# Performance work log

Measured on AMD Instinct MI355X. Metric: run time of the kernel, lower is better.

Reference implementation:

```python
import jax, jax.numpy as jnp
import numpy as np

N_HEAD = 12
TOP_M = 16
MIN_SIZE = 2
MAX_SIZE = 8
ALPHA = 1.0
EPS = 1e-6

# Note: in the torch source, minimize_det=True and minimize_det=False select the
# identical subset (the sign flip in the score is exactly undone by flipping the
# comparisons), so we implement the single equivalent rule: maximize
# s = -log(det(K_S K_S^T) + 1e-6) / |S|**alpha.

def _token(qi, i, k_all, v_all):
    """Greedy DPP subset selection for one query token i. qi:[d], k_all/v_all:[T,d]."""
    T, d = k_all.shape
    slots = jnp.arange(MAX_SIZE)
    sim = k_all @ qi
    sim = jnp.where(jnp.arange(T) <= i, sim, -jnp.inf)  # causal mask
    vals, topidx = jax.lax.top_k(sim, TOP_M)
    avail0 = jnp.isfinite(vals) & (topidx != i)  # i is removed from candidates
    k_cand = k_all[topidx]                        # [M,d]
    cand_norm = jnp.sum(k_cand * k_cand, axis=-1)  # [M]
    ki = k_all[i]
    sel0 = jnp.zeros((MAX_SIZE,), jnp.int32).at[0].set(i.astype(jnp.int32))
    s0 = jax.lax.stop_gradient(-jnp.log(jnp.dot(ki, ki) + EPS))  # |S|=1 => size^alpha=1

    def body(state, _):
        sel, count, cur_s, avail, done = state
        # E: selected key vectors in slots < count, zeros elsewhere
        E = jnp.where((slots < count)[:, None], k_all[sel], 0.0)  # [S,d]
        G0 = E @ E.T                                              # [S,S]
        cross = k_cand @ E.T  # [M,S]; column `count` is 0 since that E row is 0
        u = (slots == count).astype(E.dtype)  # one-hot insertion slot
        # Gram of S u {c} for every candidate c, identity-padded beyond slot count
        grams = (G0[None]
                 + u[None, :, None] * cross[:, None, :]
                 + cross[:, :, None] * u[None, None, :]
                 + cand_norm[:, None, None] * (u[:, None] * u[None, :])[None])
        grams = grams + jnp.diag(jnp.where(slots > count, 1.0, 0.0))[None]
        det = jnp.linalg.det(grams.astype(jnp.float32))  # [M]
        s = -jnp.log(det + EPS) / (count + 1).astype(jnp.float32) ** ALPHA
        s = jax.lax.stop_gradient(jnp.where(avail, s, -jnp.inf))
        best = jnp.argmax(s)
        best_s = s[best]
        accept = (~done) & jnp.any(avail) & ((best_s > cur_s) | (count < MIN_SIZE))
        sel = jnp.where(accept & (slots == count), topidx[best].astype(jnp.int32), sel)
        avail = avail & ~(accept & (jnp.arange(TOP_M) == best))
        cur_s = jnp.where(accept, best_s, cur_s)
        count = count + accept.astype(count.dtype)
        done = done | ~accept
        return (sel, count, cur_s, avail, done), None

    init = (sel0, jnp.int32(1), s0, avail0, jnp.bool_(False))
    (sel, count, _, _, _), _ = jax.lax.scan(body, init, None, length=MAX_SIZE - 1)
    w = (slots < count).astype(v_all.dtype)
    return (v_all[sel] * w[:, None]).sum(0) / count.astype(v_all.dtype)

_tokens = jax.vmap(_token, in_axes=(0, 0, None, None))  # over T

def _head(qh, kh, vh):
    return _tokens(qh, jnp.arange(qh.shape[0]), kh, vh)

_attn = jax.vmap(jax.vmap(_head))  # over B, H

def _forward(x, W_attn, b_attn, W_proj, b_proj):
    B, T, C = x.shape
    hs = C // N_HEAD
    qkv = x @ W_attn + b_attn
    q, k, v = jnp.split(qkv, 3, axis=-1)
    q = q.reshape(B, T, N_HEAD, hs).transpose(0, 2, 1, 3)
    k = k.reshape(B, T, N_HEAD, hs).transpose(0, 2, 1, 3)
    v = v.reshape(B, T, N_HEAD, hs).transpose(0, 2, 1, 3)
    y = _attn(q, k, v)  # [B,H,T,hs]
    y = y.transpose(0, 2, 1, 3).reshape(B, T, C)
    return y @ W_proj + b_proj  # dropout=0.0 (eval)

def setup_inputs():
    key = jax.random.key(0)
    ks = jax.random.split(key, 3)
    B, T, C = 4, 512, 768
    return {
        "x": jax.random.normal(ks[0], (B, T, C), jnp.float32),
        "W_attn": jax.random.normal(ks[1], (C, 3 * C), jnp.float32) * 0.02,
        "b_attn": jnp.zeros((3 * C,), jnp.float32),
        "W_proj": jax.random.normal(ks[2], (C, C), jnp.float32) * 0.02,
        "b_proj": jnp.zeros((C,), jnp.float32),
    }

def reference(x, W_attn, b_attn, W_proj, b_proj):
    return _forward(x, W_attn, b_attn, W_proj, b_proj)
```

## Files before the change

### kernel.cpp

```cpp
#include <hip/hip_runtime.h>
#include <math.h>

constexpr int Bc = 4, Tc = 512, Cc = 768, Hc = 12, HSc = 64;
constexpr int QKVN = 3 * Cc;
constexpr double EPSd = 1e-6;

typedef unsigned short u16;
typedef __attribute__((ext_vector_type(8))) short short8;
typedef __attribute__((ext_vector_type(4))) float f32x4;

__device__ __forceinline__ u16 f2bf(float x) {
  unsigned u = __float_as_uint(x);
  return (u16)((u + 0x7FFFu + ((u >> 16) & 1u)) >> 16);
}
__device__ __forceinline__ float bf2f(u16 h) {
  return __uint_as_float((unsigned)h << 16);
}

__device__ __forceinline__ void gload16(const u16* g, u16* l) {
  __builtin_amdgcn_global_load_lds(
      (const __attribute__((address_space(1))) void*)g,
      (__attribute__((address_space(3))) void*)l, 16, 0, 0);
}

#define WAITVM6 asm volatile("s_waitcnt vmcnt(6)" ::: "memory")
#define WAITVM0 asm volatile("s_waitcnt vmcnt(0)" ::: "memory")

__global__ void __launch_bounds__(256) convsplit3(
    const float* __restrict__ in, u16* __restrict__ H, u16* __restrict__ M,
    u16* __restrict__ L) {
  const int i = blockIdx.x * 256 + threadIdx.x;
  const float4 v = ((const float4*)in)[i];
  const float x[4] = {v.x, v.y, v.z, v.w};
  ushort4 hv, mv, lv;
  u16* hp = (u16*)&hv; u16* mp = (u16*)&mv; u16* lp = (u16*)&lv;
#pragma unroll
  for (int c = 0; c < 4; ++c) {
    const u16 h = f2bf(x[c]);
    const float r1 = x[c] - bf2f(h);
    const u16 m = f2bf(r1);
    const u16 l = f2bf(r1 - bf2f(m));
    hp[c] = h; mp[c] = m; lp[c] = l;
  }
  ((ushort4*)H)[i] = hv;
  ((ushort4*)M)[i] = mv;
  ((ushort4*)L)[i] = lv;
}

__global__ void __launch_bounds__(256) convsplit3_t(
    const float* __restrict__ W, u16* __restrict__ Th, u16* __restrict__ Tm,
    u16* __restrict__ Tl, int K, int Nn) {
  __shared__ float t[64][65];
  const int k0 = blockIdx.x * 64, n0 = blockIdx.y * 64;
#pragma unroll
  for (int u = 0; u < 16; ++u) {
    const int idx = u * 256 + threadIdx.x;
    const int r = idx >> 6, c = idx & 63;
    t[r][c] = W[(size_t)(k0 + r) * Nn + n0 + c];
  }
  __syncthreads();
#pragma unroll
  for (int u = 0; u < 16; ++u) {
    const int idx = u * 256 + threadIdx.x;
    const int n = idx >> 6, k = idx & 63;
    const float x = t[k][n];
    const u16 h = f2bf(x);
    const float r1 = x - bf2f(h);
    const u16 m = f2bf(r1);
    const u16 l = f2bf(r1 - bf2f(m));
    Th[(size_t)(n0 + n) * K + k0 + k] = h;
    Tm[(size_t)(n0 + n) * K + k0 + k] = m;
    Tl[(size_t)(n0 + n) * K + k0 + k] = l;
  }
}

template <bool WRITE_PARTIAL>
__global__ void __launch_bounds__(256, 3) gemm_mfma3(
    const u16* __restrict__ A, const u16* __restrict__ B,
    const float* __restrict__ bias, float* __restrict__ outp,
    int N, int kPerSplit, int strideA, int strideB) {
  __shared__ __align__(16) u16 AsF[2][3 * 64 * 32];
  __shared__ __align__(16) u16 BsF[2][3 * 64 * 32];
  const int tid = threadIdx.x;
  const int wid = tid >> 6;
  const int lane = tid & 63;
  const int lm = lane & 15, kg = lane >> 4;
  const int wr = wid >> 1, wc = wid & 1;
  const int rb = blockIdx.x * 64;
  const int cb = blockIdx.y * 64;
  const int kBeg = blockIdx.z * kPerSplit;

  const int trow = tid >> 2;
  const int tc4 = tid & 3;
  const int krot = ((tc4 - (trow >> 1)) & 3) * 8;
  const int sLds = tid * 8;
  int aOff = (rb + trow) * 768 + kBeg + krot;
  int bOff = (cb + trow) * 768 + kBeg + krot;

  f32x4 acc[2][2];
#pragma unroll
  for (int mf = 0; mf < 2; ++mf)
#pragma unroll
    for (int nf = 0; nf < 2; ++nf) acc[mf][nf] = (f32x4){0.f, 0.f, 0.f, 0.f};

  const int nIter = kPerSplit / 32;
  const int ckA = ((kg + (lm >> 1)) & 3) * 8;

  auto stage = [&](int buf) {
#pragma unroll
    for (int p = 0; p < 3; ++p) {
      gload16(A + (size_t)p * strideA + aOff, &AsF[buf][p * 2048 + sLds]);
      gload16(B + (size_t)p * strideB + bOff, &BsF[buf][p * 2048 + sLds]);
    }
    aOff += 32; bOff += 32;
  };
  auto compute = [&](int buf) {
    short8 ah[2], am[2], al[2];
#pragma unroll
    for (int mf = 0; mf < 2; ++mf) {
      const int ro = (wr * 32 + mf * 16 + lm) * 32 + ckA;
      ah[mf] = *(const short8*)&AsF[buf][ro];
      am[mf] = *(const short8*)&AsF[buf][2048 + ro];
      al[mf] = *(const short8*)&AsF[buf][4096 + ro];
    }
#pragma unroll
    for (int nf = 0; nf < 2; ++nf) {
      const int co = (wc * 32 + nf * 16 + lm) * 32 + ckA;
      const short8 bh = *(const short8*)&BsF[buf][co];
      const short8 bm = *(const short8*)&BsF[buf][2048 + co];
      const short8 bl = *(const short8*)&BsF[buf][4096 + co];
#pragma unroll
      for (int mf = 0; mf < 2; ++mf) {
        acc[mf][nf] = __builtin_amdgcn_mfma_f32_16x16x32_bf16(
            al[mf], bh, acc[mf][nf], 0, 0, 0);
        acc[mf][nf] = __builtin_amdgcn_mfma_f32_16x16x32_bf16(
            ah[mf], bl, acc[mf][nf], 0, 0, 0);
        acc[mf][nf] = __builtin_amdgcn_mfma_f32_16x16x32_bf16(
            am[mf], bm, acc[mf][nf], 0, 0, 0);
        acc[mf][nf] = __builtin_amdgcn_mfma_f32_16x16x32_bf16(
            am[mf], bh, acc[mf][nf], 0, 0, 0);
        acc[mf][nf] = __builtin_amdgcn_mfma_f32_16x16x32_bf16(
            ah[mf], bm, acc[mf][nf], 0, 0, 0);
        acc[mf][nf] = __builtin_amdgcn_mfma_f32_16x16x32_bf16(
            ah[mf], bh, acc[mf][nf], 0, 0, 0);
      }
    }
  };

  stage(0);
  stage(1);
  for (int t = 0; t < nIter; t += 2) {
    if (t + 1 < nIter) { WAITVM6; } else { WAITVM0; }
    __builtin_amdgcn_s_barrier();
    compute(0);
    __builtin_amdgcn_s_barrier();
    if (t + 2 < nIter) stage(0);
    if (t + 2 < nIter) { WAITVM6; } else { WAITVM0; }
    __builtin_amdgcn_s_barrier();
    compute(1);
    __builtin_amdgcn_s_barrier();
    if (t + 3 < nIter) stage(1);
  }

  const int colb = cb + wc * 32 + lm;
  if (WRITE_PARTIAL) {
    float* Pp = outp + (size_t)blockIdx.z * 2048 * N;
#pragma unroll
    for (int mf = 0; mf < 2; ++mf)
#pragma unroll
      for (int r2 = 0; r2 < 4; ++r2) {
        float* orow =
            Pp + (size_t)(rb + wr * 32 + mf * 16 + kg * 4 + r2) * N + colb;
        orow[0]  = acc[mf][0][r2];
        orow[16] = acc[mf][1][r2];
      }
  } else {
    const float bb0 = bias[colb], bb1 = bias[colb + 16];
#pragma unroll
    for (int mf = 0; mf < 2; ++mf)
#pragma unroll
      for (int r2 = 0; r2 < 4; ++r2) {
        float* orow =
            outp + (size_t)(rb + wr * 32 + mf * 16 + kg * 4 + r2) * N + colb;
        orow[0]  = acc[mf][0][r2] + bb0;
        orow[16] = acc[mf][1][r2] + bb1;
      }
  }
}

__global__ void __launch_bounds__(256) reduce_bias_kernel(
    const float* __restrict__ P, const float* __restrict__ bias,
    float* __restrict__ outp, int MN, int N, int KS) {
  const int idx4 = (blockIdx.x * 256 + threadIdx.x) * 4;
  float4 acc = *(const float4*)&P[idx4];
  for (int ks = 1; ks < KS; ++ks) {
    const float4 p = *(const float4*)&P[(size_t)ks * MN + idx4];
    acc.x += p.x; acc.y += p.y; acc.z += p.z; acc.w += p.w;
  }
  const int col = idx4 % N;
  const float4 b4 = *(const float4*)&bias[col];
  acc.x += b4.x; acc.y += b4.y; acc.z += b4.z; acc.w += b4.w;
  *(float4*)&outp[idx4] = acc;
}

__global__ void __launch_bounds__(256) sims_kernel(
    const float* __restrict__ qkv, float* __restrict__ S) {
  const int bh = blockIdx.y;
  const int b = bh / Hc, h = bh % Hc;
  int it = 0;
  {
    const int t = blockIdx.x;
    while ((it + 1) * (it + 2) / 2 <= t) ++it;
  }
  const int jt = blockIdx.x - it * (it + 1) / 2;
  const int tid = threadIdx.x;
  const int tx = tid & 15, ty = tid >> 4;
  __shared__ float Qs[HSc][68];
  __shared__ float Ks[HSc][68];
  const float* base = qkv + (size_t)b * Tc * QKVN + h * HSc;
  {
    const int row = tid >> 2;
    const int d0 = (tid & 3) * 16;
    const float* qrow = base + (size_t)(it * 64 + row) * QKVN;
    const float* krow = base + (size_t)(jt * 64 + row) * QKVN + Cc;
#pragma unroll
    for (int u = 0; u < 4; ++u) {
      const float4 q4 = *(const float4*)&qrow[d0 + u * 4];
      const float4 k4 = *(const float4*)&krow[d0 + u * 4];
      Qs[d0 + u * 4 + 0][row] = q4.x; Qs[d0 + u * 4 + 1][row] = q4.y;
      Qs[d0 + u * 4 + 2][row] = q4.z; Qs[d0 + u * 4 + 3][row] = q4.w;
      Ks[d0 + u * 4 + 0][row] = k4.x; Ks[d0 + u * 4 + 1][row] = k4.y;
      Ks[d0 + u * 4 + 2][row] = k4.z; Ks[d0 + u * 4 + 3][row] = k4.w;
    }
  }
  __syncthreads();
  float acc[4][4];
#pragma unroll
  for (int m = 0; m < 4; ++m)
#pragma unroll
    for (int n = 0; n < 4; ++n) acc[m][n] = 0.0f;
#pragma unroll 4
  for (int d = 0; d < HSc; ++d) {
    const float4 a4 = *(const float4*)&Qs[d][ty * 4];
    const float4 b4 = *(const float4*)&Ks[d][tx * 4];
    const float a[4] = {a4.x, a4.y, a4.z, a4.w};
    const float bv[4] = {b4.x, b4.y, b4.z, b4.w};
#pragma unroll
    for (int m = 0; m < 4; ++m)
#pragma unroll
      for (int n = 0; n < 4; ++n) acc[m][n] += a[m] * bv[n];
  }
  float* Shead = S + (size_t)bh * Tc * Tc;
#pragma unroll
  for (int m = 0; m < 4; ++m) {
    const int i = it * 64 + ty * 4 + m;
    float4 o4 = {acc[m][0], acc[m][1], acc[m][2], acc[m][3]};
    *(float4*)&Shead[(size_t)i * Tc + jt * 64 + tx * 4] = o4;
  }
}

__global__ void __launch_bounds__(256) topk_kernel(
    const float* __restrict__ S, int* __restrict__ topidx,
    unsigned* __restrict__ availB) {
  const int tid = threadIdx.x;
  const int wv = tid >> 6, lane = tid & 63;
  const int tok = blockIdx.x * 4 + wv;
  const int i = tok & (Tc - 1);
  const float4* Sq = reinterpret_cast<const float4*>(S + (size_t)tok * Tc);
  unsigned long long key[8];
#pragma unroll
  for (int r = 0; r < 2; ++r) {
    const float4 v4 = Sq[lane * 2 + r];
    const float vv[4] = {v4.x, v4.y, v4.z, v4.w};
#pragma unroll
    for (int c = 0; c < 4; ++c) {
      const int j = lane * 8 + r * 4 + c;
      const unsigned u = __float_as_uint(vv[c]);
      const unsigned s = (u & 0x80000000u) ? ~u : (u | 0x80000000u);
      key[r * 4 + c] = (j <= i)
          ? (((unsigned long long)s << 32) | (unsigned)(511 - j))
          : 0ull;
    }
  }
#define CE8(a, b)                                                   \
  {                                                                 \
    const unsigned long long lo_ = key[a] < key[b] ? key[a] : key[b]; \
    const unsigned long long hi_ = key[a] < key[b] ? key[b] : key[a]; \
    key[a] = hi_; key[b] = lo_;                                     \
  }
  CE8(0, 1) CE8(2, 3) CE8(0, 2) CE8(1, 3) CE8(1, 2)
  CE8(4, 5) CE8(6, 7) CE8(4, 6) CE8(5, 7) CE8(5, 6)
  CE8(0, 4) CE8(1, 5) CE8(2, 6) CE8(3, 7)
  CE8(2, 4) CE8(3, 5)
  CE8(1, 2) CE8(3, 4) CE8(5, 6)
#undef CE8

  unsigned avail = 0;
#pragma unroll
  for (int m = 0; m < 16; ++m) {
    unsigned g = (unsigned)(key[0] >> 32);
    const unsigned myhi = g;
#pragma unroll
    for (int msk = 1; msk <= 32; msk <<= 1) {
      const unsigned o = __shfl_xor(g, msk);
      g = o > g ? o : g;
    }
    const unsigned long long ball = __ballot(myhi == g);
    const int winner = __ffsll((unsigned long long)ball) - 1;
    const unsigned lo = __shfl((unsigned)key[0], winner);
    const int j = 511 - (int)lo;
    if (lane == 0) topidx[(size_t)tok * 16 + m] = j & 511;
    if (g > 0x007FFFFFu && j != i) avail |= (1u << m);
    if (lane == winner) {
      key[0] = key[1]; key[1] = key[2]; key[2] = key[3]; key[3] = key[4];
      key[4] = key[5]; key[5] = key[6]; key[6] = key[7]; key[7] = 0ull;
    }
  }
  if (lane == 0) availB[tok] = avail;
}

__global__ void __launch_bounds__(256, 4) select_kernel(
    const float* __restrict__ qkv, const int* __restrict__ topidx,
    const unsigned* __restrict__ availB, u16* __restrict__ yh,
    u16* __restrict__ ym, u16* __restrict__ yl) {
  const int tid = threadIdx.x;
  const int wv = tid >> 6, lane = tid & 63;
  const int half = lane >> 5;
  const int l32 = lane & 31;
  const int m = l32 >> 1;
  const int q = l32 & 1;
  const int hbase = half << 5;

  const int tok = blockIdx.x * 8 + wv * 2 + half;
  const int bh = tok >> 9;
  const int i = tok & (Tc - 1);
  const int b = bh / Hc;
  const int h = bh % Hc;

  const float* base = qkv + (size_t)b * Tc * QKVN + h * HSc;
  const float* kbase = base + Cc;
  const float* vbase = base + 2 * Cc;

  const int tidx = topidx[(size_t)tok * 16 + m];
  unsigned avail = availB[tok];

  float kreg[32], kireg[32];
  {
    const float* kc = kbase + (size_t)tidx * QKVN + q * 32;
    const float* ki = kbase + (size_t)i * QKVN + q * 32;
#pragma unroll
    for (int u = 0; u < 8; ++u) {
      const float4 c4 = *(const float4*)&kc[u * 4];
      const float4 i4 = *(const float4*)&ki[u * 4];
      kreg[u * 4 + 0] = c4.x; kreg[u * 4 + 1] = c4.y;
      kreg[u * 4 + 2] = c4.z; kreg[u * 4 + 3] = c4.w;
      kireg[u * 4 + 0] = i4.x; kireg[u * 4 + 1] = i4.y;
      kireg[u * 4 + 2] = i4.z; kireg[u * 4 + 3] = i4.w;
    }
  }
  float cnorm_f = 0.0f, c0_f = 0.0f, kii_f = 0.0f;
#pragma unroll
  for (int e = 0; e < 32; ++e) {
    cnorm_f += kreg[e] * kreg[e];
    c0_f += kreg[e] * kireg[e];
    kii_f += kireg[e] * kireg[e];
  }
  cnorm_f += __shfl_xor(cnorm_f, 1);
  c0_f += __shfl_xor(c0_f, 1);
  kii_f += __shfl_xor(kii_f, 1);

  const double kii = (double)kii_f;
  double z[8];
#pragma unroll
  for (int t = 0; t < 8; ++t) z[t] = 0.0;
  z[0] = (double)c0_f / sqrt(kii);
  double schur = (double)cnorm_f - z[0] * z[0];
  double detS = kii;
  double Dprev = 0.0;
  int count = 1;
  int sel[8];
  sel[0] = i;
#pragma unroll
  for (int a = 1; a < 8; ++a) sel[a] = 0;
  bool hdone = false;

#pragma unroll
  for (int it = 0; it < 7; ++it) {
    const double D = detS * schur + EPSd;
    const bool act = ((avail >> m) & 1u) != 0;
    const bool bad = !(D > 0.0);
    double dkey = act ? (bad ? -INFINITY : D) : INFINITY;
    int bm = m;
#pragma unroll
    for (int msk = 2; msk <= 16; msk <<= 1) {
      const double ok2 = __shfl_xor(dkey, msk);
      const int om = __shfl_xor(bm, msk);
      const bool t2 = (ok2 < dkey) || (ok2 == dkey && om < bm);
      dkey = t2 ? ok2 : dkey;
      bm = t2 ? om : bm;
    }
    const double Dbest = __shfl(D, hbase | (bm * 2));
    bool acc_ok;
    if (it == 0) {
      acc_ok = true;
    } else {
      double pA = Dbest, pB = Dprev;
#pragma unroll
      for (int j = 0; j < it; ++j) pA *= Dbest;
#pragma unroll
      for (int j = 0; j < it + 1; ++j) pB *= Dprev;
      acc_ok = ((avail >> bm) & 1u) && (Dbest >= 0.0) && (Dprev >= 0.0) &&
               (pA < pB);
    }
    const bool X = !hdone && (avail != 0u) && acc_ok;
    hdone = hdone || !X;
    if (X) {
      float cp_f = 0.0f;
#pragma unroll
      for (int e = 0; e < 32; ++e) {
        const float kb = __shfl(kreg[e], hbase | (bm * 2) | q);
        cp_f += kreg[e] * kb;
      }
      cp_f += __shfl_xor(cp_f, 1);
      const double schur_b = __shfl(schur, hbase | (bm * 2));
      double sum = 0.0;
#pragma unroll
      for (int t = 0; t <= it; ++t) {
        const double zbt = __shfl(z[t], hbase | (bm * 2));
        sum += z[t] * zbt;
      }
      const double znew = ((double)cp_f - sum) / sqrt(schur_b);
      z[it + 1] = znew;
      schur -= znew * znew;
      detS *= schur_b;
      Dprev = Dbest;
      avail &= ~(1u << bm);
      ++count;
      sel[it + 1] = __shfl(tidx, hbase | (bm * 2));
    }
    if (__all(hdone)) break;
  }

  double acc0 = 0.0, acc1 = 0.0;
#pragma unroll
  for (int a = 0; a < 8; ++a)
    if (a < count) {
      const float* vrow = vbase + (size_t)sel[a] * QKVN;
      acc0 += (double)vrow[l32];
      acc1 += (double)vrow[l32 + 32];
    }
  const float v0 = (float)(acc0 / (double)count);
  const float v1 = (float)(acc1 / (double)count);
  const size_t yidx = (((size_t)b * Tc + i) * Hc + h) * HSc + l32;
  {
    const u16 hv = f2bf(v0);
    const float r1 = v0 - bf2f(hv);
    const u16 mv = f2bf(r1);
    yh[yidx] = hv; ym[yidx] = mv; yl[yidx] = f2bf(r1 - bf2f(mv));
  }
  {
    const u16 hv = f2bf(v1);
    const float r1 = v1 - bf2f(hv);
    const u16 mv = f2bf(r1);
    yh[yidx + 32] = hv; ym[yidx + 32] = mv;
    yl[yidx + 32] = f2bf(r1 - bf2f(mv));
  }
}

extern "C" void kernel_launch(void* const* d_in, const int* in_sizes, int n_in,
                              void* d_out, int out_size, void* d_ws, size_t ws_size,
                              hipStream_t stream) {
  (void)in_sizes; (void)n_in; (void)out_size; (void)ws_size;
  const float* x  = (const float*)d_in[0];
  const float* Wa = (const float*)d_in[1];
  const float* ba = (const float*)d_in[2];
  const float* Wp = (const float*)d_in[3];
  const float* bp = (const float*)d_in[4];
  float* out = (float*)d_out;

  constexpr size_t XPLANE = (size_t)Bc * Tc * Cc;
  constexpr size_t WAPLANE = (size_t)QKVN * Cc;
  constexpr size_t WPPLANE = (size_t)Cc * Cc;

  float* qkv = (float*)d_ws;
  int* topidx = (int*)(qkv + (size_t)Bc * Tc * QKVN);
  unsigned* availB = (unsigned*)(topidx + (size_t)Bc * Hc * Tc * 16);
  float* regionB = (float*)(availB + (size_t)Bc * Hc * Tc);
  float* S = regionB;
  float* Pproj = regionB;
  u16* Xh = (u16*)regionB;
  u16* Wath = Xh + 3 * XPLANE;
  u16* Wpth = (u16*)(regionB + (size_t)3 * 2048 * Cc);
  u16* yhp = Wpth + 3 * WPPLANE;

  const int MNproj = Bc * Tc * Cc;

  hipLaunchKernelGGL(convsplit3, dim3(1536), dim3(256), 0, stream,
                     x, Xh, Xh + XPLANE, Xh + 2 * XPLANE);
  hipLaunchKernelGGL(convsplit3_t, dim3(12, 36), dim3(256), 0, stream,
                     Wa, Wath, Wath + WAPLANE, Wath + 2 * WAPLANE, Cc, QKVN);
  hipLaunchKernelGGL((gemm_mfma3<false>), dim3(32, QKVN / 64, 1), dim3(256),
                     0, stream, Xh, Wath, ba, qkv, QKVN, Cc,
                     (int)XPLANE, (int)WAPLANE);
  hipLaunchKernelGGL(sims_kernel, dim3(36, Bc * Hc), dim3(256), 0,
                     stream, qkv, S);
  hipLaunchKernelGGL(topk_kernel, dim3(Bc * Hc * Tc / 4), dim3(256), 0,
                     stream, S, topidx, availB);
  hipLaunchKernelGGL(select_kernel, dim3(Bc * Hc * Tc / 8), dim3(256), 0,
                     stream, qkv, topidx, availB,
                     yhp, yhp + XPLANE, yhp + 2 * XPLANE);
  hipLaunchKernelGGL(convsplit3_t, dim3(12, 12), dim3(256), 0, stream,
                     Wp, Wpth, Wpth + WPPLANE, Wpth + 2 * WPPLANE, Cc, Cc);
  hipLaunchKernelGGL((gemm_mfma3<true>), dim3(32, Cc / 64, 3), dim3(256), 0,
                     stream, yhp, Wpth, nullptr, Pproj, Cc, 256,
                     (int)XPLANE, (int)WPPLANE);
  hipLaunchKernelGGL(reduce_bias_kernel, dim3(MNproj / 1024), dim3(256), 0,
                     stream, Pproj, bp, out, MNproj, Cc, 3);
}
```

Measured before the change: 257.1 us.

## Use two-plane bf16 split for projection GEMM, swizzle tiles, skip masked topk loads

The output projection GEMM now splits its operands into two bf16 planes (high and mid) instead of three. This drops the low plane loads and three of the six MFMAs per fragment, and select_kernel no longer writes the low plane of y. Workgroup IDs in the GEMM are remapped with an XCD-style swizzle so neighbouring tiles share cache. The topk kernel also skips loading similarity scores in the causally masked region. The two-plane split lowers the precision of the projection, which could affect accuracy tolerance.

```diff
diff --git a/kernel.cpp b/kernel.cpp
--- a/kernel.cpp
+++ b/kernel.cpp
@@ -23,7 +23,6 @@
       (__attribute__((address_space(3))) void*)l, 16, 0, 0);
 }
 
-#define WAITVM6 asm volatile("s_waitcnt vmcnt(6)" ::: "memory")
 #define WAITVM0 asm volatile("s_waitcnt vmcnt(0)" ::: "memory")
 
 __global__ void __launch_bounds__(256) convsplit3(
@@ -74,20 +73,23 @@
   }
 }
 
-template <bool WRITE_PARTIAL>
+template <bool WRITE_PARTIAL, int PLANES>
 __global__ void __launch_bounds__(256, 3) gemm_mfma3(
     const u16* __restrict__ A, const u16* __restrict__ B,
     const float* __restrict__ bias, float* __restrict__ outp,
     int N, int kPerSplit, int strideA, int strideB) {
-  __shared__ __align__(16) u16 AsF[2][3 * 64 * 32];
-  __shared__ __align__(16) u16 BsF[2][3 * 64 * 32];
+  __shared__ __align__(16) u16 AsF[2][PLANES * 64 * 32];
+  __shared__ __align__(16) u16 BsF[2][PLANES * 64 * 32];
   const int tid = threadIdx.x;
   const int wid = tid >> 6;
   const int lane = tid & 63;
   const int lm = lane & 15, kg = lane >> 4;
   const int wr = wid >> 1, wc = wid & 1;
-  const int rb = blockIdx.x * 64;
-  const int cb = blockIdx.y * 64;
+  const int nwg = gridDim.x * gridDim.y;
+  const int bidl = blockIdx.x + gridDim.x * blockIdx.y;
+  const int wg = (bidl & 7) * (nwg >> 3) + (bidl >> 3);
+  const int rb = (wg % gridDim.x) * 64;
+  const int cb = (wg / gridDim.x) * 64;
   const int kBeg = blockIdx.z * kPerSplit;
 
   const int trow = tid >> 2;
@@ -106,9 +108,16 @@
   const int nIter = kPerSplit / 32;
   const int ckA = ((kg + (lm >> 1)) & 3) * 8;
 
+  auto waitN = [&]() {
+    if constexpr (PLANES == 3) {
+      asm volatile("s_waitcnt vmcnt(6)" ::: "memory");
+    } else {
+      asm volatile("s_waitcnt vmcnt(4)" ::: "memory");
+    }
+  };
   auto stage = [&](int buf) {
 #pragma unroll
-    for (int p = 0; p < 3; ++p) {
+    for (int p = 0; p < PLANES; ++p) {
       gload16(A + (size_t)p * strideA + aOff, &AsF[buf][p * 2048 + sLds]);
       gload16(B + (size_t)p * strideB + bOff, &BsF[buf][p * 2048 + sLds]);
     }
@@ -121,22 +130,25 @@
       const int ro = (wr * 32 + mf * 16 + lm) * 32 + ckA;
       ah[mf] = *(const short8*)&AsF[buf][ro];
       am[mf] = *(const short8*)&AsF[buf][2048 + ro];
-      al[mf] = *(const short8*)&AsF[buf][4096 + ro];
+      if constexpr (PLANES == 3) al[mf] = *(const short8*)&AsF[buf][4096 + ro];
     }
 #pragma unroll
     for (int nf = 0; nf < 2; ++nf) {
       const int co = (wc * 32 + nf * 16 + lm) * 32 + ckA;
       const short8 bh = *(const short8*)&BsF[buf][co];
       const short8 bm = *(const short8*)&BsF[buf][2048 + co];
-      const short8 bl = *(const short8*)&BsF[buf][4096 + co];
+      short8 bl;
+      if constexpr (PLANES == 3) bl = *(const short8*)&BsF[buf][4096 + co];
 #pragma unroll
       for (int mf = 0; mf < 2; ++mf) {
-        acc[mf][nf] = __builtin_amdgcn_mfma_f32_16x16x32_bf16(
-            al[mf], bh, acc[mf][nf], 0, 0, 0);
-        acc[mf][nf] = __builtin_amdgcn_mfma_f32_16x16x32_bf16(
-            ah[mf], bl, acc[mf][nf], 0, 0, 0);
-        acc[mf][nf] = __builtin_amdgcn_mfma_f32_16x16x32_bf16(
-            am[mf], bm, acc[mf][nf], 0, 0, 0);
+        if constexpr (PLANES == 3) {
+          acc[mf][nf] = __builtin_amdgcn_mfma_f32_16x16x32_bf16(
+              al[mf], bh, acc[mf][nf], 0, 0, 0);
+          acc[mf][nf] = __builtin_amdgcn_mfma_f32_16x16x32_bf16(
+              ah[mf], bl, acc[mf][nf], 0, 0, 0);
+          acc[mf][nf] = __builtin_amdgcn_mfma_f32_16x16x32_bf16(
+              am[mf], bm, acc[mf][nf], 0, 0, 0);
+        }
         acc[mf][nf] = __builtin_amdgcn_mfma_f32_16x16x32_bf16(
             am[mf], bh, acc[mf][nf], 0, 0, 0);
         acc[mf][nf] = __builtin_amdgcn_mfma_f32_16x16x32_bf16(
@@ -150,12 +162,12 @@
   stage(0);
   stage(1);
   for (int t = 0; t < nIter; t += 2) {
-    if (t + 1 < nIter) { WAITVM6; } else { WAITVM0; }
+    if (t + 1 < nIter) { waitN(); } else { WAITVM0; }
     __builtin_amdgcn_s_barrier();
     compute(0);
     __builtin_amdgcn_s_barrier();
     if (t + 2 < nIter) stage(0);
-    if (t + 2 < nIter) { WAITVM6; } else { WAITVM0; }
+    if (t + 2 < nIter) { waitN(); } else { WAITVM0; }
     __builtin_amdgcn_s_barrier();
     compute(1);
     __builtin_amdgcn_s_barrier();
@@ -270,16 +282,22 @@
   unsigned long long key[8];
 #pragma unroll
   for (int r = 0; r < 2; ++r) {
-    const float4 v4 = Sq[lane * 2 + r];
-    const float vv[4] = {v4.x, v4.y, v4.z, v4.w};
-#pragma unroll
-    for (int c = 0; c < 4; ++c) {
-      const int j = lane * 8 + r * 4 + c;
-      const unsigned u = __float_as_uint(vv[c]);
-      const unsigned s = (u & 0x80000000u) ? ~u : (u | 0x80000000u);
-      key[r * 4 + c] = (j <= i)
-          ? (((unsigned long long)s << 32) | (unsigned)(511 - j))
-          : 0ull;
+    const int jb = lane * 8 + r * 4;
+    if (jb <= i) {
+      const float4 v4 = Sq[lane * 2 + r];
+      const float vv[4] = {v4.x, v4.y, v4.z, v4.w};
+#pragma unroll
+      for (int c = 0; c < 4; ++c) {
+        const int j = jb + c;
+        const unsigned u = __float_as_uint(vv[c]);
+        const unsigned s = (u & 0x80000000u) ? ~u : (u | 0x80000000u);
+        key[r * 4 + c] = (j <= i)
+            ? (((unsigned long long)s << 32) | (unsigned)(511 - j))
+            : 0ull;
+      }
+    } else {
+      key[r * 4 + 0] = 0ull; key[r * 4 + 1] = 0ull;
+      key[r * 4 + 2] = 0ull; key[r * 4 + 3] = 0ull;
     }
   }
 #define CE8(a, b)                                                   \
@@ -322,7 +340,7 @@
 __global__ void __launch_bounds__(256, 4) select_kernel(
     const float* __restrict__ qkv, const int* __restrict__ topidx,
     const unsigned* __restrict__ availB, u16* __restrict__ yh,
-    u16* __restrict__ ym, u16* __restrict__ yl) {
+    u16* __restrict__ ym) {
   const int tid = threadIdx.x;
   const int wv = tid >> 6, lane = tid & 63;
   const int half = lane >> 5;
@@ -454,16 +472,11 @@
   const size_t yidx = (((size_t)b * Tc + i) * Hc + h) * HSc + l32;
   {
     const u16 hv = f2bf(v0);
-    const float r1 = v0 - bf2f(hv);
-    const u16 mv = f2bf(r1);
-    yh[yidx] = hv; ym[yidx] = mv; yl[yidx] = f2bf(r1 - bf2f(mv));
+    yh[yidx] = hv; ym[yidx] = f2bf(v0 - bf2f(hv));
   }
   {
     const u16 hv = f2bf(v1);
-    const float r1 = v1 - bf2f(hv);
-    const u16 mv = f2bf(r1);
-    yh[yidx + 32] = hv; ym[yidx + 32] = mv;
-    yl[yidx + 32] = f2bf(r1 - bf2f(mv));
+    yh[yidx + 32] = hv; ym[yidx + 32] = f2bf(v1 - bf2f(hv));
   }
 }
 
@@ -499,20 +512,19 @@
                      x, Xh, Xh + XPLANE, Xh + 2 * XPLANE);
   hipLaunchKernelGGL(convsplit3_t, dim3(12, 36), dim3(256), 0, stream,
                      Wa, Wath, Wath + WAPLANE, Wath + 2 * WAPLANE, Cc, QKVN);
-  hipLaunchKernelGGL((gemm_mfma3<false>), dim3(32, QKVN / 64, 1), dim3(256),
-                     0, stream, Xh, Wath, ba, qkv, QKVN, Cc,
+  hipLaunchKernelGGL((gemm_mfma3<false, 3>), dim3(32, QKVN / 64, 1),
+                     dim3(256), 0, stream, Xh, Wath, ba, qkv, QKVN, Cc,
                      (int)XPLANE, (int)WAPLANE);
   hipLaunchKernelGGL(sims_kernel, dim3(36, Bc * Hc), dim3(256), 0,
                      stream, qkv, S);
   hipLaunchKernelGGL(topk_kernel, dim3(Bc * Hc * Tc / 4), dim3(256), 0,
                      stream, S, topidx, availB);
   hipLaunchKernelGGL(select_kernel, dim3(Bc * Hc * Tc / 8), dim3(256), 0,
-                     stream, qkv, topidx, availB,
-                     yhp, yhp + XPLANE, yhp + 2 * XPLANE);
+                     stream, qkv, topidx, availB, yhp, yhp + XPLANE);
   hipLaunchKernelGGL(convsplit3_t, dim3(12, 12), dim3(256), 0, stream,
                      Wp, Wpth, Wpth + WPPLANE, Wpth + 2 * WPPLANE, Cc, Cc);
-  hipLaunchKernelGGL((gemm_mfma3<true>), dim3(32, Cc / 64, 3), dim3(256), 0,
-                     stream, yhp, Wpth, nullptr, Pproj, Cc, 256,
+  hipLaunchKernelGGL((gemm_mfma3<true, 2>), dim3(32, Cc / 64, 3), dim3(256),
+                     0, stream, yhp, Wpth, nullptr, Pproj, Cc, 256,
                      (int)XPLANE, (int)WPPLANE);
   hipLaunchKernelGGL(reduce_bias_kernel, dim3(MNproj / 1024), dim3(256), 0,
                      stream, Pproj, bp, out, MNproj, Cc, 3);
```

Result: slower. 264.2 us (+2.8%).
